# Kernel tuning notes

Measured on AMD Instinct MI355X. Metric: run time of the kernel, lower is better.

Reference implementation:

```python
import jax, jax.numpy as jnp
import numpy as np

N_DEST, N_SRC = 8192, 8192
FEAT, TFD, EMB, HID, HEADS = 1024, 256, 64, 128, 2
NEG_INF = -9e15


def setup_inputs() -> dict:
    key = jax.random.key(0)
    ks = jax.random.split(key, 8)
    bias = (jax.random.uniform(ks[0], (N_DEST, N_SRC)) < 0.01).astype(jnp.float32)
    emb_dest = jax.random.normal(ks[1], (N_DEST, EMB), jnp.float32)
    emb_src = jax.random.normal(ks[2], (N_SRC, EMB), jnp.float32)
    feature_src = jax.random.normal(ks[3], (N_SRC, FEAT), jnp.float32)
    scale = 0.05
    fc_W = jax.random.normal(ks[4], (TFD, FEAT), jnp.float32) * scale
    fc_b = jnp.zeros((TFD,), jnp.float32)
    dec_W = jax.random.normal(ks[5], (FEAT, TFD), jnp.float32) * scale
    dec_b = jnp.zeros((FEAT,), jnp.float32)
    att_W = jax.random.normal(ks[6], (HEADS, EMB, HID), jnp.float32) * scale
    att_W2 = jax.random.normal(ks[7], (HEADS, HID, HID), jnp.float32) * scale
    return dict(bias=bias, emb_dest=emb_dest, emb_src=emb_src,
                feature_src=feature_src, fc_W=fc_W, fc_b=fc_b,
                dec_W=dec_W, dec_b=dec_b, att_W=att_W, att_W2=att_W2)


def reference(bias, emb_dest, emb_src, feature_src, fc_W, fc_b, dec_W, dec_b, att_W, att_W2):
    # encoder: [N_src, FEAT] -> [N_src, TFD]
    transformed = feature_src @ fc_W.T + fc_b
    # per-head projections of node embeddings: h = emb @ W  -> [H, N, HID]
    h_src = jnp.einsum('ne,hed->hnd', emb_src, att_W)
    h_dst = jnp.einsum('me,hed->hmd', emb_dest, att_W)
    # e = elu((h_dst @ W2) @ h_src^T)  -> [H, N_dest, N_src]
    scores = jax.nn.elu(jnp.einsum('hmd,hdk,hnk->hmn', h_dst, att_W2, h_src))
    masked = jnp.where(bias > 0, scores, NEG_INF)
    attn = jax.nn.softmax(masked, axis=-1)  # row-wise over source nodes
    # aggregate transformed source features, mean over heads -> [N_dest, TFD]
    feature_src_re = jnp.einsum('hmn,nf->hmf', attn, transformed).mean(axis=0)
    # decoder (autoencoder reconstruction): [N_src, FEAT]
    feature_hat = transformed @ dec_W.T + dec_b
    return feature_src_re, feature_hat
```

## Files before the change

### kernel.cpp

```cpp
#include <hip/hip_runtime.h>
#include <hip/hip_bf16.h>

#define N_DEST 8192
#define N_SRC  8192
#define FEATD  1024
#define TFDIM  256
#define EMBD   64
#define HIDD   128
#define LDO    1024
#define LSTRIDE 256
#define SCAP 240

typedef float  f32x4  __attribute__((ext_vector_type(4)));
typedef __bf16 bf16x8 __attribute__((ext_vector_type(8)));
typedef unsigned short u16x4 __attribute__((ext_vector_type(4)));

__device__ inline bf16x8 load8cvt(const float* p) {
  const f32x4 u = *(const f32x4*)p;
  const f32x4 v = *(const f32x4*)(p + 4);
  bf16x8 r;
  #pragma unroll
  for (int i = 0; i < 4; ++i) { r[i] = (__bf16)u[i]; r[i + 4] = (__bf16)v[i]; }
  return r;
}
__device__ inline unsigned short bfbits(float f) {
  __bf16 b = (__bf16)f;
  return *(unsigned short*)&b;
}
__device__ inline float bf2f(unsigned short u) {
  union { unsigned int i; float f; } x;
  x.i = (unsigned int)u << 16;
  return x.f;
}

__global__ __launch_bounds__(256) void cvt_weights(
    const float* __restrict__ fc_W, const float* __restrict__ dec_W,
    unsigned short* __restrict__ wpack, unsigned short* __restrict__ dpack)
{
  const int which = blockIdx.x >> 8;
  const int i = ((blockIdx.x & 255) * 256 + threadIdx.x) * 4;
  const float* src = which ? dec_W : fc_W;
  unsigned short* dst = which ? dpack : wpack;
  const f32x4 v = *(const f32x4*)(src + i);
  u16x4 o;
  #pragma unroll
  for (int e = 0; e < 4; ++e) o[e] = bfbits(v[e]);
  *(u16x4*)(dst + i) = o;
}

__global__ __launch_bounds__(256) void gemm_mfma_k1(
    const float* __restrict__ A, const float* __restrict__ B,
    const float* __restrict__ bias, float* __restrict__ stage,
    unsigned short* __restrict__ apack,
    const unsigned short* __restrict__ wpack)
{
  const int wave = threadIdx.x >> 6, lane = threadIdx.x & 63;
  const int l15 = lane & 15, quad = lane >> 4;
  const int row0 = blockIdx.x * 64 + wave * 16;
  const int col0 = blockIdx.y * 64;

  const float* Ap = A + (size_t)(row0 + l15) * FEATD + quad * 8;

  f32x4 acc[4];
  #pragma unroll
  for (int i = 0; i < 4; ++i) acc[i] = (f32x4){0.f, 0.f, 0.f, 0.f};

  if (wpack) {
    const unsigned short* Bq = wpack + (size_t)(col0 + l15) * FEATD + quad * 8;
    for (int k = 0; k < FEATD; k += 32) {
      const bf16x8 a  = load8cvt(Ap + k);
      const bf16x8 b0 = *(const bf16x8*)(Bq + k);
      const bf16x8 b1 = *(const bf16x8*)(Bq + (size_t)16 * FEATD + k);
      const bf16x8 b2 = *(const bf16x8*)(Bq + (size_t)32 * FEATD + k);
      const bf16x8 b3 = *(const bf16x8*)(Bq + (size_t)48 * FEATD + k);
      acc[0] = __builtin_amdgcn_mfma_f32_16x16x32_bf16(a, b0, acc[0], 0, 0, 0);
      acc[1] = __builtin_amdgcn_mfma_f32_16x16x32_bf16(a, b1, acc[1], 0, 0, 0);
      acc[2] = __builtin_amdgcn_mfma_f32_16x16x32_bf16(a, b2, acc[2], 0, 0, 0);
      acc[3] = __builtin_amdgcn_mfma_f32_16x16x32_bf16(a, b3, acc[3], 0, 0, 0);
    }
  } else {
    const float* Bp = B + (size_t)(col0 + l15) * FEATD + quad * 8;
    for (int k = 0; k < FEATD; k += 32) {
      const bf16x8 a  = load8cvt(Ap + k);
      const bf16x8 b0 = load8cvt(Bp + k);
      const bf16x8 b1 = load8cvt(Bp + (size_t)16 * FEATD + k);
      const bf16x8 b2 = load8cvt(Bp + (size_t)32 * FEATD + k);
      const bf16x8 b3 = load8cvt(Bp + (size_t)48 * FEATD + k);
      acc[0] = __builtin_amdgcn_mfma_f32_16x16x32_bf16(a, b0, acc[0], 0, 0, 0);
      acc[1] = __builtin_amdgcn_mfma_f32_16x16x32_bf16(a, b1, acc[1], 0, 0, 0);
      acc[2] = __builtin_amdgcn_mfma_f32_16x16x32_bf16(a, b2, acc[2], 0, 0, 0);
      acc[3] = __builtin_amdgcn_mfma_f32_16x16x32_bf16(a, b3, acc[3], 0, 0, 0);
    }
  }

  #pragma unroll
  for (int ct = 0; ct < 4; ++ct) {
    const int n = col0 + ct * 16 + l15;
    const float bn = bias[n];
    #pragma unroll
    for (int r = 0; r < 4; ++r) {
      const int mm = row0 + quad * 4 + r;
      const float v = acc[ct][r] + bn;
      const unsigned short pb = bfbits(v);
      stage[(size_t)mm * LDO + n] = v;
      ((unsigned short*)(stage + (size_t)mm * LDO + 768))[n] = pb;
      if (apack) apack[(size_t)mm * TFDIM + n] = pb;
    }
  }
}

__global__ __launch_bounds__(128) void proj_all(
    const float* __restrict__ emb_src, const float* __restrict__ emb_dest,
    const float* __restrict__ att_W, const float* __restrict__ att_W2,
    float* __restrict__ stage)
{
  const int t = threadIdx.x;
  const int b = blockIdx.x;
  const int rb    = b & 511;
  const int h     = (b >> 9) & 1;
  const int which = b >> 10;
  const int row0  = rb * 16;

  __shared__ float se[16][EMBD];
  __shared__ float hh[16][HIDD];

  const float* e = (which ? emb_dest : emb_src) + (size_t)row0 * EMBD;
  for (int i = t; i < 16 * EMBD; i += 128) se[i >> 6][i & 63] = e[i];
  __syncthreads();

  float acc[16];
  #pragma unroll
  for (int r = 0; r < 16; ++r) acc[r] = 0.f;
  const float* W = att_W + (size_t)h * EMBD * HIDD + t;
  for (int d = 0; d < EMBD; ++d) {
    const float w = W[d * HIDD];
    #pragma unroll
    for (int r = 0; r < 16; ++r) acc[r] += se[r][d] * w;
  }

  if (!which) {
    #pragma unroll
    for (int r = 0; r < 16; ++r) {
      const size_t row = row0 + r;
      stage[row * LDO + 256 + h * HIDD + t] = acc[r];
      ((unsigned short*)(stage + row * LDO + 896))[h * HIDD + t] = bfbits(acc[r]);
    }
    return;
  }

  #pragma unroll
  for (int r = 0; r < 16; ++r) hh[r][t] = acc[r];
  __syncthreads();

  float g[16];
  #pragma unroll
  for (int r = 0; r < 16; ++r) g[r] = 0.f;
  const float* W2 = att_W2 + (size_t)h * HIDD * HIDD + t;
  for (int d = 0; d < HIDD; ++d) {
    const float w2 = W2[d * HIDD];
    #pragma unroll
    for (int r = 0; r < 16; ++r) g[r] += hh[r][d] * w2;
  }
  #pragma unroll
  for (int r = 0; r < 16; ++r)
    stage[(size_t)(row0 + r) * LDO + 512 + h * HIDD + t] = g[r];
}

__global__ __launch_bounds__(256) void extract_nbrs(
    const float* __restrict__ bias, int* __restrict__ counts,
    int* __restrict__ lists)
{
  const int m = blockIdx.x;
  const int tid = threadIdx.x, lane = tid & 63;
  __shared__ int cnt;
  if (tid == 0) cnt = 0;
  __syncthreads();
  const float* brow = bias + (size_t)m * N_SRC;
  int* lrow = lists + (size_t)m * LSTRIDE;
  for (int base = tid * 4; base < N_SRC; base += 1024) {
    const f32x4 v = *(const f32x4*)(brow + base);
    #pragma unroll
    for (int e = 0; e < 4; ++e) {
      const bool nz = v[e] > 0.f;
      const unsigned long long msk = __ballot(nz);
      int wbase = 0;
      if (lane == 0 && msk) wbase = atomicAdd(&cnt, __popcll(msk));
      wbase = __shfl(wbase, 0);
      if (nz) {
        const int p = wbase + __popcll(msk & ((1ull << lane) - 1ull));
        if (p < LSTRIDE) lrow[p] = base + e;
      }
    }
  }
  __syncthreads();
  if (tid == 0) counts[m] = cnt;
}

__global__ __launch_bounds__(256, 4) void attn_gather(
    const float* __restrict__ bias, const float* __restrict__ stage,
    const int* __restrict__ counts, const int* __restrict__ lists,
    float* __restrict__ out)
{
  const int m = blockIdx.x;
  const int tid = threadIdx.x;
  const int lane = tid & 63, wv = tid >> 6;

  __shared__ float gq[4][68];
  __shared__ float s0[256], s1[256];
  __shared__ int   lidx[256];
  __shared__ float rA[4], rB[4];
  __shared__ float p0[4][TFDIM], p1[4][TFDIM];

  const float* gs = stage + (size_t)m * LDO + 512;
  gq[wv][lane] = gs[(wv >> 1) * HIDD + (wv & 1) * 64 + lane];
  const int count = counts[m];
  __syncthreads();

  if (count > 0 && count <= SCAP) {
    const int countPad = (count + 15) & ~15;
    if (tid < countPad)
      lidx[tid] = (tid < count) ? lists[(size_t)m * LSTRIDE + tid] : 0;
    __syncthreads();

    const int grp = tid >> 2, r4 = tid & 3;
    const int h = r4 >> 1, half = r4 & 1;
    const float* gh = gq[r4];
    for (int t0 = 0; t0 < count; t0 += 64) {
      const int t = t0 + grp;
      float q = 0.f;
      if (t < count) {
        const int j = lidx[t];
        const __bf16* hb =
            (const __bf16*)(stage + (size_t)j * LDO + 896) + h * HIDD + half * 64;
        #pragma unroll
        for (int s = 0; s < 8; ++s) {
          const bf16x8 x = *(const bf16x8*)(hb + s * 8);
          #pragma unroll
          for (int e = 0; e < 8; ++e) q += gh[s * 8 + e] * (float)x[e];
        }
      }
      q += __shfl_xor(q, 1);
      if (t < count && half == 0) {
        const float sc = (q > 0.f) ? q : expm1f(q);
        if (h == 0) s0[t] = sc; else s1[t] = sc;
      }
    }
    __syncthreads();

    float m0 = (tid < count) ? s0[tid] : -3.4e38f;
    float m1 = (tid < count) ? s1[tid] : -3.4e38f;
    #pragma unroll
    for (int off = 32; off; off >>= 1) {
      m0 = fmaxf(m0, __shfl_xor(m0, off));
      m1 = fmaxf(m1, __shfl_xor(m1, off));
    }
    if (lane == 0) { rA[wv] = m0; rB[wv] = m1; }
    __syncthreads();
    const float M0 = fmaxf(fmaxf(rA[0], rA[1]), fmaxf(rA[2], rA[3]));
    const float M1 = fmaxf(fmaxf(rB[0], rB[1]), fmaxf(rB[2], rB[3]));
    __syncthreads();

    float w0 = 0.f, w1 = 0.f;
    if (tid < count) {
      w0 = __expf(s0[tid] - M0);
      w1 = __expf(s1[tid] - M1);
    }
    if (tid < countPad) { s0[tid] = w0; s1[tid] = w1; }
    float l0 = w0, l1 = w1;
    #pragma unroll
    for (int off = 32; off; off >>= 1) {
      l0 += __shfl_xor(l0, off);
      l1 += __shfl_xor(l1, off);
    }
    if (lane == 0) { rA[wv] = l0; rB[wv] = l1; }
    __syncthreads();
    const float L0 = rA[0] + rA[1] + rA[2] + rA[3];
    const float L1 = rB[0] + rB[1] + rB[2] + rB[3];

    float b0[4] = {0.f, 0.f, 0.f, 0.f};
    float b1[4] = {0.f, 0.f, 0.f, 0.f};
    const int c4 = lane << 2;
    for (int t = wv << 2; t < countPad; t += 16) {
      #pragma unroll
      for (int q = 0; q < 4; ++q) {
        const int j = lidx[t + q];
        const float u0 = s0[t + q], u1 = s1[t + q];
        const u16x4 tv = *(const u16x4*)(
            (const unsigned short*)(stage + (size_t)j * LDO + 768) + c4);
        #pragma unroll
        for (int i = 0; i < 4; ++i) {
          const float f = bf2f(tv[i]);
          b0[i] += u0 * f;
          b1[i] += u1 * f;
        }
      }
    }
    #pragma unroll
    for (int i = 0; i < 4; ++i) {
      p0[wv][c4 + i] = b0[i];
      p1[wv][c4 + i] = b1[i];
    }
    __syncthreads();
    const float A0 = p0[0][tid] + p0[1][tid] + p0[2][tid] + p0[3][tid];
    const float A1 = p1[0][tid] + p1[1][tid] + p1[2][tid] + p1[3][tid];
    out[(size_t)m * TFDIM + tid] = 0.5f * (A0 / L0 + A1 / L1);
    return;
  }

  float* w0s = (float*)p0[0];
  float* w1s = (float*)p0[1];
  const int c = tid;
  float a0 = 0.f, a1 = 0.f;
  float M0 = -3.4e38f, M1 = -3.4e38f, L0 = 0.f, L1 = 0.f;
  for (int j0 = 0; j0 < N_SRC; j0 += 256) {
    const int j = j0 + tid;
    const float* hb = stage + (size_t)j * LDO + 256;
    float q0 = 0.f, q1 = 0.f;
    for (int d = 0; d < HIDD; d += 4) {
      const int hf = d >> 6, dd = d & 63;
      const f32x4 x = *(const f32x4*)(hb + d);
      const f32x4 y = *(const f32x4*)(hb + HIDD + d);
      #pragma unroll
      for (int e = 0; e < 4; ++e) {
        q0 += gq[hf][dd + e] * x[e];
        q1 += gq[2 + hf][dd + e] * y[e];
      }
    }
    const bool nz = bias[(size_t)m * N_SRC + j] > 0.f;
    const float sc0 = nz ? ((q0 > 0.f) ? q0 : expm1f(q0)) : -9e15f;
    const float sc1 = nz ? ((q1 > 0.f) ? q1 : expm1f(q1)) : -9e15f;

    float cm0 = sc0, cm1 = sc1;
    #pragma unroll
    for (int off = 32; off; off >>= 1) {
      cm0 = fmaxf(cm0, __shfl_xor(cm0, off));
      cm1 = fmaxf(cm1, __shfl_xor(cm1, off));
    }
    if (lane == 0) { rA[wv] = cm0; rB[wv] = cm1; }
    __syncthreads();
    const float CM0 = fmaxf(fmaxf(rA[0], rA[1]), fmaxf(rA[2], rA[3]));
    const float CM1 = fmaxf(fmaxf(rB[0], rB[1]), fmaxf(rB[2], rB[3]));
    __syncthreads();

    const float nM0 = fmaxf(M0, CM0), nM1 = fmaxf(M1, CM1);
    const float r0 = __expf(M0 - nM0), r1 = __expf(M1 - nM1);
    const float w0 = __expf(sc0 - nM0), w1 = __expf(sc1 - nM1);
    w0s[tid] = w0; w1s[tid] = w1;
    float cl0 = w0, cl1 = w1;
    #pragma unroll
    for (int off = 32; off; off >>= 1) {
      cl0 += __shfl_xor(cl0, off);
      cl1 += __shfl_xor(cl1, off);
    }
    if (lane == 0) { rA[wv] = cl0; rB[wv] = cl1; }
    __syncthreads();
    L0 = L0 * r0 + (rA[0] + rA[1] + rA[2] + rA[3]);
    L1 = L1 * r1 + (rB[0] + rB[1] + rB[2] + rB[3]);
    M0 = nM0; M1 = nM1;
    a0 *= r0; a1 *= r1;
    for (int t2 = 0; t2 < 256; ++t2) {
      const float tv = stage[(size_t)(j0 + t2) * LDO + c];
      a0 += w0s[t2] * tv;
      a1 += w1s[t2] * tv;
    }
    __syncthreads();
  }
  out[(size_t)m * TFDIM + c] = 0.5f * (a0 / L0 + a1 / L1);
}

__global__ __launch_bounds__(64) void attn_stream(
    const float* __restrict__ bias, const float* __restrict__ stage,
    float* __restrict__ out)
{
  const int lane = threadIdx.x;
  const int m = blockIdx.x;
  const int c0 = lane * 4;

  __shared__ float g0[HIDD], g1[HIDD];
  __shared__ int   ring[256];
  __shared__ float wb0[64], wb1[64];

  const float* gs = stage + (size_t)m * LDO + 512;
  g0[lane]      = gs[lane];
  g0[lane + 64] = gs[lane + 64];
  g1[lane]      = gs[HIDD + lane];
  g1[lane + 64] = gs[HIDD + lane + 64];
  __syncthreads();

  float O0[4] = {0.f, 0.f, 0.f, 0.f};
  float O1[4] = {0.f, 0.f, 0.f, 0.f};
  float M0 = -3.4e38f, M1 = -3.4e38f;
  float L0 = 0.f, L1 = 0.f;

  auto flush = [&](int b, int rp) {
    __syncthreads();
    int j = -1;
    if (lane < b) j = ring[(rp + lane) & 255];
    float s0 = 0.f, s1 = 0.f;
    if (j >= 0) {
      const float* h0 = stage + (size_t)j * LDO + 256;
      const float* h1 = h0 + HIDD;
      #pragma unroll
      for (int d = 0; d < HIDD; d += 4) {
        const f32x4 a = *(const f32x4*)(h0 + d);
        const f32x4 c = *(const f32x4*)(h1 + d);
        #pragma unroll
        for (int e = 0; e < 4; ++e) {
          s0 += g0[d + e] * a[e];
          s1 += g1[d + e] * c[e];
        }
      }
      s0 = (s0 > 0.f) ? s0 : expm1f(s0);
      s1 = (s1 > 0.f) ? s1 : expm1f(s1);
    }
    float m0 = (j >= 0) ? s0 : -3.4e38f;
    float m1 = (j >= 0) ? s1 : -3.4e38f;
    #pragma unroll
    for (int off = 32; off; off >>= 1) {
      m0 = fmaxf(m0, __shfl_xor(m0, off));
      m1 = fmaxf(m1, __shfl_xor(m1, off));
    }
    const float nM0 = fmaxf(M0, m0), nM1 = fmaxf(M1, m1);
    const float w0 = (j >= 0) ? __expf(s0 - nM0) : 0.f;
    const float w1 = (j >= 0) ? __expf(s1 - nM1) : 0.f;
    float l0 = w0, l1 = w1;
    #pragma unroll
    for (int off = 32; off; off >>= 1) {
      l0 += __shfl_xor(l0, off);
      l1 += __shfl_xor(l1, off);
    }
    const float r0 = __expf(M0 - nM0);
    const float r1 = __expf(M1 - nM1);
    L0 = L0 * r0 + l0;  L1 = L1 * r1 + l1;
    M0 = nM0;  M1 = nM1;
    #pragma unroll
    for (int i = 0; i < 4; ++i) { O0[i] *= r0; O1[i] *= r1; }
    wb0[lane] = w0;  wb1[lane] = w1;
    __syncthreads();
    for (int n = 0; n < b; ++n) {
      const int jj = ring[(rp + n) & 255];
      const float wa = wb0[n], wc = wb1[n];
      const f32x4 tv = *(const f32x4*)(stage + (size_t)jj * LDO + c0);
      #pragma unroll
      for (int i = 0; i < 4; ++i) {
        O0[i] += wa * tv[i];
        O1[i] += wc * tv[i];
      }
    }
    __syncthreads();
  };

  const float* brow = bias + (size_t)m * N_SRC;
  int wpos = 0, rpos = 0;
  for (int base = 0; base < N_SRC; base += 256) {
    const f32x4 v = *(const f32x4*)(brow + base + lane * 4);
    #pragma unroll
    for (int e = 0; e < 4; ++e) {
      const bool nz = v[e] > 0.f;
      const unsigned long long mask = __ballot(nz);
      if (nz) {
        const int pos = wpos + __popcll(mask & ((1ull << lane) - 1ull));
        ring[pos & 255] = base + lane * 4 + e;
      }
      wpos += __popcll(mask);
      if (wpos - rpos >= 64) { flush(64, rpos); rpos += 64; }
    }
  }
  while (wpos - rpos > 0) {
    const int b = (wpos - rpos < 64) ? (wpos - rpos) : 64;
    flush(b, rpos);
    rpos += b;
  }

  float* orow = out + (size_t)m * TFDIM + c0;
  if (wpos == 0) {
    float o[4] = {0.f, 0.f, 0.f, 0.f};
    for (int j = 0; j < N_SRC; ++j) {
      const f32x4 tv = *(const f32x4*)(stage + (size_t)j * LDO + c0);
      #pragma unroll
      for (int i = 0; i < 4; ++i) o[i] += tv[i];
    }
    const float inv = 1.f / (float)N_SRC;
    #pragma unroll
    for (int i = 0; i < 4; ++i) orow[i] = o[i] * inv;
  } else {
    const float i0 = 1.f / L0, i1 = 1.f / L1;
    #pragma unroll
    for (int i = 0; i < 4; ++i)
      orow[i] = 0.5f * (O0[i] * i0 + O1[i] * i1);
  }
}

__global__ __launch_bounds__(256) void gemm_mfma_dec2(
    const unsigned short* __restrict__ apack,
    const unsigned short* __restrict__ dpack,
    const float* __restrict__ bias,
    float* __restrict__ OUT)
{
  const int wave = threadIdx.x >> 6, lane = threadIdx.x & 63;
  const int l15 = lane & 15, quad = lane >> 4;
  const int row0 = blockIdx.x * 64 + wave * 16;
  const int col0 = blockIdx.y * 64;

  const unsigned short* Ap = apack + (size_t)(row0 + l15) * TFDIM + quad * 8;
  const unsigned short* Bp = dpack + (size_t)(col0 + l15) * TFDIM + quad * 8;

  f32x4 acc[4];
  #pragma unroll
  for (int i = 0; i < 4; ++i) acc[i] = (f32x4){0.f, 0.f, 0.f, 0.f};

  #pragma unroll
  for (int k = 0; k < TFDIM; k += 32) {
    const bf16x8 a  = *(const bf16x8*)(Ap + k);
    const bf16x8 b0 = *(const bf16x8*)(Bp + k);
    const bf16x8 b1 = *(const bf16x8*)(Bp + (size_t)16 * TFDIM + k);
    const bf16x8 b2 = *(const bf16x8*)(Bp + (size_t)32 * TFDIM + k);
    const bf16x8 b3 = *(const bf16x8*)(Bp + (size_t)48 * TFDIM + k);
    acc[0] = __builtin_amdgcn_mfma_f32_16x16x32_bf16(a, b0, acc[0], 0, 0, 0);
    acc[1] = __builtin_amdgcn_mfma_f32_16x16x32_bf16(a, b1, acc[1], 0, 0, 0);
    acc[2] = __builtin_amdgcn_mfma_f32_16x16x32_bf16(a, b2, acc[2], 0, 0, 0);
    acc[3] = __builtin_amdgcn_mfma_f32_16x16x32_bf16(a, b3, acc[3], 0, 0, 0);
  }

  #pragma unroll
  for (int ct = 0; ct < 4; ++ct) {
    const int n = col0 + ct * 16 + l15;
    const float bn = bias[n];
    #pragma unroll
    for (int r = 0; r < 4; ++r) {
      const int mm = row0 + quad * 4 + r;
      OUT[(size_t)mm * LDO + n] = acc[ct][r] + bn;
    }
  }
}

__global__ __launch_bounds__(128) void gemm_mfma_dec(
    const float* __restrict__ W,
    const float* __restrict__ bias,
    float* __restrict__ OUT)
{
  const int row0 = blockIdx.x * 32;
  const int tid = threadIdx.x;
  const int wave = tid >> 6, lane = tid & 63;
  const int l15 = lane & 15, quad = lane >> 4;

  __shared__ __bf16 Ab[32][TFDIM + 8];

  for (int i = tid; i < 32 * TFDIM; i += 128) {
    const int r = i >> 8, k = i & 255;
    Ab[r][k] = (__bf16)OUT[(size_t)(row0 + r) * LDO + k];
  }
  __syncthreads();

  bf16x8 af[8];
  #pragma unroll
  for (int ks = 0; ks < 8; ++ks)
    af[ks] = *(const bf16x8*)&Ab[wave * 16 + l15][ks * 32 + quad * 8];

  for (int ct = 0; ct < 16; ++ct) {
    f32x4 acc[4];
    #pragma unroll
    for (int i = 0; i < 4; ++i) acc[i] = (f32x4){0.f, 0.f, 0.f, 0.f};
    #pragma unroll
    for (int ks = 0; ks < 8; ++ks) {
      #pragma unroll
      for (int cg = 0; cg < 4; ++cg) {
        const int n = ct * 64 + cg * 16 + l15;
        const bf16x8 bf = load8cvt(W + (size_t)n * TFDIM + ks * 32 + quad * 8);
        acc[cg] = __builtin_amdgcn_mfma_f32_16x16x32_bf16(af[ks], bf, acc[cg], 0, 0, 0);
      }
    }
    #pragma unroll
    for (int cg = 0; cg < 4; ++cg) {
      const int n = ct * 64 + cg * 16 + l15;
      const float bn = bias[n];
      #pragma unroll
      for (int r = 0; r < 4; ++r) {
        const int mm = row0 + wave * 16 + quad * 4 + r;
        OUT[(size_t)mm * LDO + n] = acc[cg][r] + bn;
      }
    }
  }
}

extern "C" void kernel_launch(void* const* d_in, const int* in_sizes, int n_in,
                              void* d_out, int out_size, void* d_ws, size_t ws_size,
                              hipStream_t stream) {
  const float* bias        = (const float*)d_in[0];
  const float* emb_dest    = (const float*)d_in[1];
  const float* emb_src     = (const float*)d_in[2];
  const float* feature_src = (const float*)d_in[3];
  const float* fc_W        = (const float*)d_in[4];
  const float* fc_b        = (const float*)d_in[5];
  const float* dec_W       = (const float*)d_in[6];
  const float* dec_b       = (const float*)d_in[7];
  const float* att_W       = (const float*)d_in[8];
  const float* att_W2      = (const float*)d_in[9];

  float* out0 = (float*)d_out;
  float* out1 = out0 + (size_t)N_DEST * TFDIM;

  const size_t lists_bytes = (size_t)N_DEST * LSTRIDE * sizeof(int);
  const size_t apack_bytes = (size_t)N_SRC * TFDIM * sizeof(unsigned short);
  const size_t wpack_bytes = (size_t)TFDIM * FEATD * sizeof(unsigned short);
  const size_t dpack_bytes = (size_t)FEATD * TFDIM * sizeof(unsigned short);
  const size_t need = 65536 + lists_bytes + apack_bytes + wpack_bytes + dpack_bytes;
  const bool use_ws = (ws_size >= need);
  int* counts = (int*)d_ws;
  int* lists  = (int*)((char*)d_ws + 65536);
  unsigned short* apack = (unsigned short*)((char*)d_ws + 65536 + lists_bytes);
  unsigned short* wpack = (unsigned short*)((char*)apack + apack_bytes);
  unsigned short* dpack = (unsigned short*)((char*)wpack + wpack_bytes);

  if (use_ws)
    cvt_weights<<<512, 256, 0, stream>>>(fc_W, dec_W, wpack, dpack);

  if (use_ws)
    extract_nbrs<<<N_DEST, 256, 0, stream>>>(bias, counts, lists);

  {
    dim3 grid(N_SRC / 64, TFDIM / 64);
    gemm_mfma_k1<<<grid, 256, 0, stream>>>(
        feature_src, fc_W, fc_b, out1,
        use_ws ? apack : (unsigned short*)nullptr,
        use_ws ? wpack : (const unsigned short*)nullptr);
  }
  proj_all<<<2048, 128, 0, stream>>>(emb_src, emb_dest, att_W, att_W2, out1);
  if (use_ws) {
    attn_gather<<<N_DEST, 256, 0, stream>>>(bias, out1, counts, lists, out0);
  } else {
    attn_stream<<<N_DEST, 64, 0, stream>>>(bias, out1, out0);
  }
  if (use_ws) {
    dim3 grid(N_SRC / 64, FEATD / 64);
    gemm_mfma_dec2<<<grid, 256, 0, stream>>>(apack, dpack, dec_b, out1);
  } else {
    gemm_mfma_dec<<<N_SRC / 32, 128, 0, stream>>>(dec_W, dec_b, out1);
  }
}
```

Measured before the change: 645.5 us.

## Fuse neighbor extraction into attention kernel and pack bf16 operands densely

Merges the separate neighbor-list extraction kernel into the attention gather kernel, so each row's adjacency indices are built directly in shared memory instead of being written to and reread from global lists and counts. The bf16 copies of the transformed features and source projections move from strided slots inside the 1024-wide staging rows to dense 256-wide packed buffers, so gathers touch contiguous, smaller rows. This removes one launch and the global round trip of lists, at the cost of a larger fused kernel whose occupancy hint changes from 4 to 6 blocks.

```diff
diff --git a/kernel.cpp b/kernel.cpp
--- a/kernel.cpp
+++ b/kernel.cpp
@@ -8,7 +8,6 @@
 #define EMBD   64
 #define HIDD   128
 #define LDO    1024
-#define LSTRIDE 256
 #define SCAP 240
 
 typedef float  f32x4  __attribute__((ext_vector_type(4)));
@@ -101,10 +100,8 @@
     for (int r = 0; r < 4; ++r) {
       const int mm = row0 + quad * 4 + r;
       const float v = acc[ct][r] + bn;
-      const unsigned short pb = bfbits(v);
       stage[(size_t)mm * LDO + n] = v;
-      ((unsigned short*)(stage + (size_t)mm * LDO + 768))[n] = pb;
-      if (apack) apack[(size_t)mm * TFDIM + n] = pb;
+      if (apack) apack[(size_t)mm * TFDIM + n] = bfbits(v);
     }
   }
 }
@@ -112,7 +109,7 @@
 __global__ __launch_bounds__(128) void proj_all(
     const float* __restrict__ emb_src, const float* __restrict__ emb_dest,
     const float* __restrict__ att_W, const float* __restrict__ att_W2,
-    float* __restrict__ stage)
+    float* __restrict__ stage, unsigned short* __restrict__ hpack)
 {
   const int t = threadIdx.x;
   const int b = blockIdx.x;
@@ -143,7 +140,7 @@
     for (int r = 0; r < 16; ++r) {
       const size_t row = row0 + r;
       stage[row * LDO + 256 + h * HIDD + t] = acc[r];
-      ((unsigned short*)(stage + row * LDO + 896))[h * HIDD + t] = bfbits(acc[r]);
+      if (hpack) hpack[row * TFDIM + h * HIDD + t] = bfbits(acc[r]);
     }
     return;
   }
@@ -166,17 +163,29 @@
     stage[(size_t)(row0 + r) * LDO + 512 + h * HIDD + t] = g[r];
 }
 
-__global__ __launch_bounds__(256) void extract_nbrs(
-    const float* __restrict__ bias, int* __restrict__ counts,
-    int* __restrict__ lists)
+__global__ __launch_bounds__(256, 6) void attn_fused(
+    const float* __restrict__ bias, const float* __restrict__ stage,
+    const unsigned short* __restrict__ hpack,
+    const unsigned short* __restrict__ apack,
+    float* __restrict__ out)
 {
   const int m = blockIdx.x;
-  const int tid = threadIdx.x, lane = tid & 63;
-  __shared__ int cnt;
+  const int tid = threadIdx.x;
+  const int lane = tid & 63, wv = tid >> 6;
+
+  __shared__ float gq[4][68];
+  __shared__ float s0[256], s1[256];
+  __shared__ int   lidx[256];
+  __shared__ float rA[4], rB[4];
+  __shared__ float p0[4][TFDIM], p1[4][TFDIM];
+  __shared__ int   cnt;
+
+  const float* gs = stage + (size_t)m * LDO + 512;
+  gq[wv][lane] = gs[(wv >> 1) * HIDD + (wv & 1) * 64 + lane];
   if (tid == 0) cnt = 0;
   __syncthreads();
+
   const float* brow = bias + (size_t)m * N_SRC;
-  int* lrow = lists + (size_t)m * LSTRIDE;
   for (int base = tid * 4; base < N_SRC; base += 1024) {
     const f32x4 v = *(const f32x4*)(brow + base);
     #pragma unroll
@@ -188,38 +197,16 @@
       wbase = __shfl(wbase, 0);
       if (nz) {
         const int p = wbase + __popcll(msk & ((1ull << lane) - 1ull));
-        if (p < LSTRIDE) lrow[p] = base + e;
+        if (p < 256) lidx[p] = base + e;
       }
     }
   }
   __syncthreads();
-  if (tid == 0) counts[m] = cnt;
-}
-
-__global__ __launch_bounds__(256, 4) void attn_gather(
-    const float* __restrict__ bias, const float* __restrict__ stage,
-    const int* __restrict__ counts, const int* __restrict__ lists,
-    float* __restrict__ out)
-{
-  const int m = blockIdx.x;
-  const int tid = threadIdx.x;
-  const int lane = tid & 63, wv = tid >> 6;
-
-  __shared__ float gq[4][68];
-  __shared__ float s0[256], s1[256];
-  __shared__ int   lidx[256];
-  __shared__ float rA[4], rB[4];
-  __shared__ float p0[4][TFDIM], p1[4][TFDIM];
-
-  const float* gs = stage + (size_t)m * LDO + 512;
-  gq[wv][lane] = gs[(wv >> 1) * HIDD + (wv & 1) * 64 + lane];
-  const int count = counts[m];
-  __syncthreads();
+  const int count = cnt;
 
   if (count > 0 && count <= SCAP) {
     const int countPad = (count + 15) & ~15;
-    if (tid < countPad)
-      lidx[tid] = (tid < count) ? lists[(size_t)m * LSTRIDE + tid] : 0;
+    if (tid >= count && tid < countPad) lidx[tid] = 0;
     __syncthreads();
 
     const int grp = tid >> 2, r4 = tid & 3;
@@ -231,7 +218,7 @@
       if (t < count) {
         const int j = lidx[t];
         const __bf16* hb =
-            (const __bf16*)(stage + (size_t)j * LDO + 896) + h * HIDD + half * 64;
+            (const __bf16*)hpack + (size_t)j * TFDIM + h * HIDD + half * 64;
         #pragma unroll
         for (int s = 0; s < 8; ++s) {
           const bf16x8 x = *(const bf16x8*)(hb + s * 8);
@@ -285,8 +272,7 @@
       for (int q = 0; q < 4; ++q) {
         const int j = lidx[t + q];
         const float u0 = s0[t + q], u1 = s1[t + q];
-        const u16x4 tv = *(const u16x4*)(
-            (const unsigned short*)(stage + (size_t)j * LDO + 768) + c4);
+        const u16x4 tv = *(const u16x4*)(apack + (size_t)j * TFDIM + c4);
         #pragma unroll
         for (int i = 0; i < 4; ++i) {
           const float f = bf2f(tv[i]);
@@ -600,23 +586,19 @@
   float* out0 = (float*)d_out;
   float* out1 = out0 + (size_t)N_DEST * TFDIM;
 
-  const size_t lists_bytes = (size_t)N_DEST * LSTRIDE * sizeof(int);
   const size_t apack_bytes = (size_t)N_SRC * TFDIM * sizeof(unsigned short);
   const size_t wpack_bytes = (size_t)TFDIM * FEATD * sizeof(unsigned short);
   const size_t dpack_bytes = (size_t)FEATD * TFDIM * sizeof(unsigned short);
-  const size_t need = 65536 + lists_bytes + apack_bytes + wpack_bytes + dpack_bytes;
-  const bool use_ws = (ws_size >= need);
-  int* counts = (int*)d_ws;
-  int* lists  = (int*)((char*)d_ws + 65536);
-  unsigned short* apack = (unsigned short*)((char*)d_ws + 65536 + lists_bytes);
-  unsigned short* wpack = (unsigned short*)((char*)apack + apack_bytes);
+  const size_t hpack_bytes = (size_t)N_SRC * TFDIM * sizeof(unsigned short);
+  const bool use_ws =
+      (ws_size >= apack_bytes + wpack_bytes + dpack_bytes + hpack_bytes);
+  unsigned short* apack = (unsigned short*)d_ws;
+  unsigned short* wpack = (unsigned short*)((char*)d_ws + apack_bytes);
   unsigned short* dpack = (unsigned short*)((char*)wpack + wpack_bytes);
+  unsigned short* hpack = (unsigned short*)((char*)dpack + dpack_bytes);
 
   if (use_ws)
     cvt_weights<<<512, 256, 0, stream>>>(fc_W, dec_W, wpack, dpack);
-
-  if (use_ws)
-    extract_nbrs<<<N_DEST, 256, 0, stream>>>(bias, counts, lists);
 
   {
     dim3 grid(N_SRC / 64, TFDIM / 64);
@@ -625,9 +607,10 @@
         use_ws ? apack : (unsigned short*)nullptr,
         use_ws ? wpack : (const unsigned short*)nullptr);
   }
-  proj_all<<<2048, 128, 0, stream>>>(emb_src, emb_dest, att_W, att_W2, out1);
+  proj_all<<<2048, 128, 0, stream>>>(emb_src, emb_dest, att_W, att_W2, out1,
+                                     use_ws ? hpack : (unsigned short*)nullptr);
   if (use_ws) {
-    attn_gather<<<N_DEST, 256, 0, stream>>>(bias, out1, counts, lists, out0);
+    attn_fused<<<N_DEST, 256, 0, stream>>>(bias, out1, hpack, apack, out0);
   } else {
     attn_stream<<<N_DEST, 64, 0, stream>>>(bias, out1, out0);
   }
```

Result: faster. 628.7 us (-2.6%).
